# Kernel tuning notes

Hardware: AMD Instinct MI355X
Metric: run time of the kernel (lower is better)

The kernel has to match this reference:

```python
import jax, jax.numpy as jnp
import numpy as np
from jax import lax

NH = 8
DK = 64
DV = 64
IN_C = 64
OUT_C = 128
FH = 32
FW = 32


def conv2d(x, w, b, pad):
    y = lax.conv_general_dilated(x, w, window_strides=(1, 1),
                                 padding=[(pad, pad), (pad, pad)],
                                 dimension_numbers=('NCHW', 'OIHW', 'NCHW'))
    return y + b[None, :, None, None]


def conv1x1(x, w, b):
    # w: [O, C, 1, 1]
    y = jnp.einsum('bchw,oc->bohw', x, w[:, :, 0, 0])
    return y + b[None, :, None, None]


def rel_to_abs(x):
    # x: [B, N, L, 2L-1] -> [B, N, L, L]
    b, n, L, _ = x.shape
    x = jnp.pad(x, ((0, 0), (0, 0), (0, 0), (0, 1)))          # [B,N,L,2L]
    flat = x.reshape(b, n, L * 2 * L)
    flat = jnp.pad(flat, ((0, 0), (0, 0), (0, L - 1)))
    final = flat.reshape(b, n, L + 1, 2 * L - 1)
    return final[:, :, :L, L - 1:]


def relative_logits_1d(q, rel_k, perm):
    # q: [B, Nh, H, W, d]; rel_k: [2W-1, d]
    b, nh, H, W, _ = q.shape
    rel = jnp.einsum('bnxyd,md->bnxym', q, rel_k)              # [B,Nh,H,W,2W-1]
    rel = rel_to_abs(rel.reshape(b, nh * H, W, 2 * W - 1))     # [B,Nh*H,W,W]
    rel = rel.reshape(b, nh, H, 1, W, W)
    rel = jnp.broadcast_to(rel, (b, nh, H, H, W, W))
    rel = jnp.transpose(rel, perm)
    return rel.reshape(b, nh, H * W, H * W)


def augmented_forward(x, conv_w, conv_b, qkv_w, qkv_b, attn_w, attn_b,
                      key_rel_w, key_rel_h):
    b, c, h, w = x.shape
    dkh = DK // NH
    dvh = DV // NH
    hw = h * w

    conv_out = conv2d(x, conv_w, conv_b, pad=1)                # [B, OUT_C-DV, H, W]

    qkv = conv1x1(x, qkv_w, qkv_b)                             # [B, 2DK+DV, H, W]
    q, k, v = jnp.split(qkv, [DK, 2 * DK], axis=1)
    q = q.reshape(b, NH, dkh, h, w) * (dkh ** -0.5)
    k = k.reshape(b, NH, dkh, h, w)
    v = v.reshape(b, NH, dvh, h, w)

    flat_q = q.reshape(b, NH, dkh, hw)
    flat_k = k.reshape(b, NH, dkh, hw)
    flat_v = v.reshape(b, NH, dvh, hw)

    logits = jnp.einsum('bndi,bndj->bnij', flat_q, flat_k)     # [B,Nh,hw,hw]

    q_bnhwd = jnp.transpose(q, (0, 1, 3, 4, 2))                # [B,Nh,H,W,d]
    # width: [B,Nh,H,W,W] broadcast over h2 -> perm to [B,Nh,h,w,h2,w2]
    logits = logits + relative_logits_1d(q_bnhwd, key_rel_w, (0, 1, 2, 4, 3, 5))
    # height: transpose H<->W, perm to [B,Nh,h,w,h2,w2]
    q_t = jnp.transpose(q_bnhwd, (0, 1, 3, 2, 4))
    logits = logits + relative_logits_1d(q_t, key_rel_h, (0, 1, 4, 2, 5, 3))

    weights = jax.nn.softmax(logits, axis=-1)
    attn_out = jnp.einsum('bnij,bndj->bnid', weights, flat_v)  # [B,Nh,hw,dvh]
    attn_out = jnp.transpose(attn_out, (0, 1, 3, 2)).reshape(b, DV, h, w)
    attn_out = conv1x1(attn_out, attn_w, attn_b)
    return jnp.concatenate([conv_out, attn_out], axis=1)


def setup_inputs() -> dict:
    key = jax.random.key(0)
    ks = jax.random.split(key, 10)
    dkh = DK // NH
    return {
        'x': jax.random.normal(ks[0], (8, IN_C, FH, FW), jnp.float32),
        'conv_w': jax.random.normal(ks[1], (OUT_C - DV, IN_C, 3, 3), jnp.float32) * 0.05,
        'conv_b': jnp.zeros((OUT_C - DV,), jnp.float32),
        'qkv_w': jax.random.normal(ks[2], (2 * DK + DV, IN_C, 1, 1), jnp.float32) * 0.05,
        'qkv_b': jnp.zeros((2 * DK + DV,), jnp.float32),
        'attn_w': jax.random.normal(ks[3], (DV, DV, 1, 1), jnp.float32) * 0.05,
        'attn_b': jnp.zeros((DV,), jnp.float32),
        'key_rel_w': jax.random.normal(ks[4], (2 * FW - 1, dkh), jnp.float32) + DK ** -0.5,
        'key_rel_h': jax.random.normal(ks[5], (2 * FH - 1, dkh), jnp.float32) + DK ** -0.5,
    }


def reference(x, conv_w, conv_b, qkv_w, qkv_b, attn_w, attn_b, key_rel_w, key_rel_h):
    return augmented_forward(x, conv_w, conv_b, qkv_w, qkv_b, attn_w, attn_b,
                             key_rel_w, key_rel_h)
```

## Files before the change

kernel.cpp:

```cpp
#include <hip/hip_runtime.h>
#include <hip/hip_bf16.h>
#include <hip/hip_fp16.h>


constexpr int QBUF  = 0;
constexpr int KVBUF = 524288;
constexpr int APRE  = KVBUF + 524288;
constexpr int XT    = APRE + 524288;
constexpr int WT    = XT + 262144;

typedef _Float16 f16x4 __attribute__((ext_vector_type(4)));
typedef _Float16 f16x8 __attribute__((ext_vector_type(8)));
typedef float f32x4 __attribute__((ext_vector_type(4)));

__device__ __forceinline__ float fexp2(float x) {
#if defined(__has_builtin) && __has_builtin(__builtin_amdgcn_exp2f)
    return __builtin_amdgcn_exp2f(x);
#else
    return exp2f(x);
#endif
}

__device__ __forceinline__ float dot8(float4 a, float4 b, const float* r) {
    return a.x*r[0] + a.y*r[1] + a.z*r[2] + a.w*r[3] +
           b.x*r[4] + b.y*r[5] + b.z*r[6] + b.w*r[7];
}

__device__ __forceinline__ f32x4 mfma16x16x32f16(f16x8 a, f16x8 b, f32x4 c) {
    return __builtin_amdgcn_mfma_f32_16x16x32_f16(a, b, c, 0, 0, 0);
}

__device__ __forceinline__ f32x4 mfma16x16x16f16(f16x4 a, f16x4 b, f32x4 c) {
    return __builtin_amdgcn_mfma_f32_16x16x16f16(a, b, c, 0, 0, 0);
}

union PK16 { __half2 hh; unsigned int u; };
union F16V { uint4 u; f16x8 h; };
union F16V4 { uint2 u; f16x4 h; };

constexpr float QSCALE = 0.35355339059327373f * 1.4426950408889634f;

__global__ __launch_bounds__(256) void k_qkv(
    const float* __restrict__ x,
    const float* __restrict__ wq,
    const float* __restrict__ bq,
    const float* __restrict__ wconv,
    float* __restrict__ qbuf,
    unsigned int* __restrict__ kvh,
    unsigned short* __restrict__ xt,
    __half* __restrict__ wt)
{
    int blk = blockIdx.x;
    int tid = threadIdx.x;

    if (blk < 16) {
        int oc0 = blk * 4;
        const float* src = wconv + oc0 * 576;
        #pragma unroll
        for (int j = 0; j < 9; ++j) {
            int local = tid + j * 256;
            float v = src[local];
            int ocr = local / 576, rem = local % 576;
            int ic = rem / 9, tap = rem % 9;
            wt[(oc0 + ocr) * 576 + tap * 64 + ic] = __float2half_rn(v);
        }
        return;
    }

    __shared__ __align__(16) float4 wl4[192];
    __shared__ float bl[12];

    int mblk = blk - 16;
    int b = mblk >> 6, rem = mblk & 63, pc = rem >> 4, og = rem & 15;

    if (tid < 192) wl4[tid] = ((const float4*)(wq + og * 768))[tid];
    if (tid < 12)  bl[tid] = bq[og * 12 + tid];

    int p = pc * 256 + tid;
    const float* xb = x + (b * 64) * 1024 + p;
    float xr[64];
    #pragma unroll
    for (int c = 0; c < 64; ++c) xr[c] = xb[c * 1024];

    __syncthreads();

    for (int pr = 0; pr < 6; ++pr) {
        int oo = pr * 2;
        float accA = bl[oo], accB = bl[oo + 1];
        #pragma unroll
        for (int c4 = 0; c4 < 16; ++c4) {
            float4 wa = wl4[oo * 16 + c4];
            float4 wb = wl4[(oo + 1) * 16 + c4];
            accA = fmaf(wa.x, xr[c4 * 4 + 0], accA);
            accA = fmaf(wa.y, xr[c4 * 4 + 1], accA);
            accA = fmaf(wa.z, xr[c4 * 4 + 2], accA);
            accA = fmaf(wa.w, xr[c4 * 4 + 3], accA);
            accB = fmaf(wb.x, xr[c4 * 4 + 0], accB);
            accB = fmaf(wb.y, xr[c4 * 4 + 1], accB);
            accB = fmaf(wb.z, xr[c4 * 4 + 2], accB);
            accB = fmaf(wb.w, xr[c4 * 4 + 3], accB);
        }
        int o = og * 12 + oo;
        if (o < 64) {
            float2 qv = make_float2(accA * QSCALE, accB * QSCALE);
            *(float2*)(qbuf + ((b * 8 + (o >> 3)) * 1024 + p) * 8 + (o & 7)) = qv;
        } else {
            PK16 pk;
            pk.hh = __floats2half2_rn(accA, accB);
            int idx;
            if (o < 128) {
                int kk = o - 64;
                idx = ((b * 8 + (kk >> 3)) * 1024 + p) * 8 + ((kk & 7) >> 1);
            } else {
                int vv = o - 128;
                idx = ((b * 8 + (vv >> 3)) * 1024 + p) * 8 + 4 + ((vv & 7) >> 1);
            }
            kvh[idx] = pk.u;
        }
    }

    if (og == 0) {
        unsigned int px[32];
        #pragma unroll
        for (int i = 0; i < 32; ++i) {
            PK16 pk;
            pk.hh = __floats2half2_rn(xr[2 * i], xr[2 * i + 1]);
            px[i] = pk.u;
        }
        uint4* dst = (uint4*)(xt + ((size_t)b * 1024 + p) * 64);
        #pragma unroll
        for (int j = 0; j < 8; ++j)
            dst[j] = make_uint4(px[4 * j], px[4 * j + 1], px[4 * j + 2], px[4 * j + 3]);
    }
}

__global__ __launch_bounds__(256) void k_attn(
    const float* __restrict__ qbuf,
    const unsigned int* __restrict__ kvh,
    const float* __restrict__ relw,
    const float* __restrict__ relh,
    float* __restrict__ apre)
{
    __shared__ __align__(16) unsigned char smem[45280];
    unsigned short* Vt  = (unsigned short*)smem;
    unsigned short* Kl  = (unsigned short*)(smem + 18656);
    _Float16*       AHS = (_Float16*)(smem + 35040);

    int tid = threadIdx.x;
    int lane = tid & 63, wv = tid >> 6;
    int bn = blockIdx.x >> 3, qc = blockIdx.x & 7;
    int b = bn >> 3, nh = bn & 7;

    {
        const uint4* kvsrc = (const uint4*)kvh + bn * 2048;
        int p0 = tid * 4;
        #pragma unroll
        for (int pp = 0; pp < 2; ++pp) {
            int pa = p0 + pp * 2;
            uint4 ka = kvsrc[pa * 2 + 0], va = kvsrc[pa * 2 + 1];
            uint4 kb = kvsrc[pa * 2 + 2], vb = kvsrc[pa * 2 + 3];
            *(uint4*)(Kl + pa * 8) = ka;
            *(uint4*)(Kl + pa * 8 + 8) = kb;
            const unsigned short* ha = (const unsigned short*)&va;
            const unsigned short* hb = (const unsigned short*)&vb;
            #pragma unroll
            for (int dv = 0; dv < 8; ++dv) {
                unsigned int pk = (unsigned int)ha[dv] | ((unsigned int)hb[dv] << 16);
                *(unsigned int*)(Vt + dv * 1036 + pa) = pk;
            }
        }
        *(unsigned long long*)(Vt + 8 * 1036 + tid * 4) = 0x3C003C003C003C00ull;
    }

    {
        int qloc = tid >> 1, hh = (tid & 1) * 16;
        int q = qc * 128 + qloc;
        const float* qp = qbuf + (bn * 1024 + q) * 8;
        float4 qa = *(const float4*)qp, qb2 = *(const float4*)(qp + 4);
        int hq = q >> 5;
        #pragma unroll
        for (int m = 0; m < 16; ++m)
            AHS[qloc * 40 + hh + m] =
                (_Float16)dot8(qa, qb2, relh + (hh + m + 31 - hq) * 8);
    }

    int r = lane & 15, g = lane >> 4;
    int qrow0 = wv * 32;
    f16x8 qf[2];
    float awE[2][4], awO[2][4];
    #pragma unroll
    for (int qt = 0; qt < 2; ++qt) {
        int qrow = qrow0 + qt * 16 + r;
        const float* qp = qbuf + (bn * 1024 + qc * 128 + qrow) * 8;
        float4 qa = *(const float4*)qp;
        float4 qb2 = *(const float4*)(qp + 4);
        f16x8 v = {0, 0, 0, 0, 0, 0, 0, 0};
        if (g == 0) {
            v[0] = (_Float16)qa.x; v[1] = (_Float16)qa.y;
            v[2] = (_Float16)qa.z; v[3] = (_Float16)qa.w;
            v[4] = (_Float16)qb2.x; v[5] = (_Float16)qb2.y;
            v[6] = (_Float16)qb2.z; v[7] = (_Float16)qb2.w;
        }
        qf[qt] = v;
        int wq = qrow & 31;
        #pragma unroll
        for (int j = 0; j < 4; ++j) {
            awE[qt][j] = dot8(qa, qb2, relw + (g * 4 + j + 31 - wq) * 8);
            awO[qt][j] = dot8(qa, qb2, relw + (16 + g * 4 + j + 31 - wq) * 8);
        }
    }

    __syncthreads();

    f32x4 acc2[2] = {{0.f, 0.f, 0.f, 0.f}, {0.f, 0.f, 0.f, 0.f}};
    const f32x4 zero = {0.f, 0.f, 0.f, 0.f};

    #pragma unroll 2
    for (int ktp = 0; ktp < 32; ++ktp) {
        int kt0 = ktp * 2;
        F16V kf0, kf1; F16V4 vt0, vt1;
        kf0.u = *(const uint4*)(Kl + (kt0 * 16 + r) * 8);
        kf1.u = *(const uint4*)(Kl + (kt0 * 16 + 16 + r) * 8);
        vt0.u = *(const uint2*)(Vt + r * 1036 + kt0 * 16 + g * 4);
        vt1.u = *(const uint2*)(Vt + r * 1036 + kt0 * 16 + 16 + g * 4);
        #pragma unroll
        for (int qt = 0; qt < 2; ++qt) {
            int qrow = qrow0 + qt * 16 + r;
            float ah = (float)AHS[qrow * 40 + ktp];
            f32x4 a1 = mfma16x16x32f16(kf0.h, qf[qt], zero);
            float e0 = fexp2(a1[0] + awE[qt][0] + ah);
            float e1 = fexp2(a1[1] + awE[qt][1] + ah);
            float e2 = fexp2(a1[2] + awE[qt][2] + ah);
            float e3 = fexp2(a1[3] + awE[qt][3] + ah);
            f16x4 pf;
            pf[0] = (_Float16)e0; pf[1] = (_Float16)e1;
            pf[2] = (_Float16)e2; pf[3] = (_Float16)e3;
            acc2[qt] = mfma16x16x16f16(vt0.h, pf, acc2[qt]);

            f32x4 a2 = mfma16x16x32f16(kf1.h, qf[qt], zero);
            float o0 = fexp2(a2[0] + awO[qt][0] + ah);
            float o1 = fexp2(a2[1] + awO[qt][1] + ah);
            float o2 = fexp2(a2[2] + awO[qt][2] + ah);
            float o3 = fexp2(a2[3] + awO[qt][3] + ah);
            f16x4 pg;
            pg[0] = (_Float16)o0; pg[1] = (_Float16)o1;
            pg[2] = (_Float16)o2; pg[3] = (_Float16)o3;
            acc2[qt] = mfma16x16x16f16(vt1.h, pg, acc2[qt]);
        }
    }

    #pragma unroll
    for (int qt = 0; qt < 2; ++qt) {
        float lsum = __shfl(acc2[qt][0], 32 + r, 64);
        float inv = 1.0f / lsum;
        if (g < 2) {
            int qglob = qc * 128 + qrow0 + qt * 16 + r;
            float* ap = apre + (b * 64 + nh * 8 + g * 4) * 1024 + qglob;
            ap[0]    = acc2[qt][0] * inv;
            ap[1024] = acc2[qt][1] * inv;
            ap[2048] = acc2[qt][2] * inv;
            ap[3072] = acc2[qt][3] * inv;
        }
    }
}

__global__ __launch_bounds__(256) void k_out(
    const unsigned short* __restrict__ xt,
    const unsigned short* __restrict__ wt,
    const float* __restrict__ bconv,
    const float* __restrict__ wattn,
    const float* __restrict__ battn,
    const float* __restrict__ apre,
    float* __restrict__ out)
{
    __shared__ __align__(16) float smem[4352];
    int blk = blockIdx.x;
    int tid = threadIdx.x;

    if (blk < 128) {
        int b = blk >> 4;
        int r0 = (blk & 15) * 2;
        int p0 = r0 * 32;
        int lane = tid & 63, wv = tid >> 6;
        int lr = lane & 15, lk = lane >> 4;
        int n0 = wv * 16;

        F16V bw[18];
        {
            const uint4* wp = (const uint4*)(wt + (n0 + lr) * 576 + lk * 8);
            #pragma unroll
            for (int kk = 0; kk < 18; ++kk) bw[kk].u = wp[kk * 4];
        }

        unsigned char* ats = (unsigned char*)smem;
        {
            const uint4* xsrc = (const uint4*)xt + b * 8192;
            #pragma unroll
            for (int it = 0; it < 5; ++it) {
                int chunk = tid + it * 256;
                if (chunk < 1088) {
                    int s = chunk & 7, cpos = chunk >> 3;
                    int sr = cpos / 34, sc = cpos - sr * 34;
                    int ir = r0 - 1 + sr, icc = sc - 1;
                    uint4 v = make_uint4(0u, 0u, 0u, 0u);
                    if (((unsigned)ir < 32u) && ((unsigned)icc < 32u))
                        v = xsrc[(ir * 32 + icc) * 8 + s];
                    int db = ((sr * 34 + sc) * 128 + s * 16) ^ ((sc & 7) << 4);
                    *(uint4*)(ats + db) = v;
                }
            }
        }
        __syncthreads();

        f32x4 acc[4];
        #pragma unroll
        for (int mb = 0; mb < 4; ++mb) acc[mb] = f32x4{0.f, 0.f, 0.f, 0.f};

        #pragma unroll
        for (int kk = 0; kk < 18; ++kk) {
            const int tap = kk >> 1, h = kk & 1;
            const int dr = tap / 3, dc = tap - dr * 3;
            #pragma unroll
            for (int mb = 0; mb < 4; ++mb) {
                int m = mb * 16 + lr;
                int sr = (m >> 5) + dr, sc = (m & 31) + dc;
                int db = ((sr * 34 + sc) * 128 + h * 64 + lk * 16) ^ ((sc & 7) << 4);
                F16V av;
                av.u = *(const uint4*)(ats + db);
                acc[mb] = __builtin_amdgcn_mfma_f32_16x16x32_f16(av.h, bw[kk].h, acc[mb], 0, 0, 0);
            }
        }

        __syncthreads();
        #pragma unroll
        for (int mb = 0; mb < 4; ++mb) {
            #pragma unroll
            for (int rr = 0; rr < 4; ++rr)
                smem[(mb * 16 + lk * 4 + rr) * 65 + n0 + lr] = acc[mb][rr];
        }
        __syncthreads();

        int oc = tid >> 2, pq = tid & 3;
        float bia = bconv[oc];
        float* op = out + ((b * 128 + oc) * 1024) + p0 + pq * 16;
        #pragma unroll
        for (int j4 = 0; j4 < 4; ++j4) {
            int mloc = pq * 16 + j4 * 4;
            float4 o4;
            o4.x = smem[(mloc + 0) * 65 + oc] + bia;
            o4.y = smem[(mloc + 1) * 65 + oc] + bia;
            o4.z = smem[(mloc + 2) * 65 + oc] + bia;
            o4.w = smem[(mloc + 3) * 65 + oc] + bia;
            *(float4*)(op + j4 * 4) = o4;
        }
    } else {
        int pb = blk - 128;
        int b = pb >> 5, rem = pb & 31, rg = rem >> 3, og = rem & 7;
        int o0 = og * 8;
        float* wl = smem;
        for (int i = tid; i < 512; i += 256) {
            int g = i & 7, c = i >> 3;
            wl[c * 8 + g] = wattn[(o0 + g) * 64 + c];
        }
        if (tid < 8) smem[512 + tid] = battn[o0 + tid];
        __syncthreads();

        int p = rg * 256 + tid;
        float acc[8] = {0, 0, 0, 0, 0, 0, 0, 0};
        const float* ap = apre + b * 65536 + p;
        #pragma unroll 16
        for (int c = 0; c < 64; ++c) {
            float xv = ap[c * 1024];
            const float4* wv4 = (const float4*)(wl + c * 8);
            float4 wa = wv4[0], wb = wv4[1];
            acc[0] = fmaf(wa.x, xv, acc[0]); acc[1] = fmaf(wa.y, xv, acc[1]);
            acc[2] = fmaf(wa.z, xv, acc[2]); acc[3] = fmaf(wa.w, xv, acc[3]);
            acc[4] = fmaf(wb.x, xv, acc[4]); acc[5] = fmaf(wb.y, xv, acc[5]);
            acc[6] = fmaf(wb.z, xv, acc[6]); acc[7] = fmaf(wb.w, xv, acc[7]);
        }
        #pragma unroll
        for (int g = 0; g < 8; ++g)
            out[(b * 128 + 64 + o0 + g) * 1024 + p] = acc[g] + smem[512 + g];
    }
}

extern "C" void kernel_launch(void* const* d_in, const int* in_sizes, int n_in,
                              void* d_out, int out_size, void* d_ws, size_t ws_size,
                              hipStream_t stream)
{
    float* ws = (float*)d_ws;
    float* out = (float*)d_out;
    const float* x      = (const float*)d_in[0];
    const float* conv_w = (const float*)d_in[1];
    const float* conv_b = (const float*)d_in[2];
    const float* qkv_w  = (const float*)d_in[3];
    const float* qkv_b  = (const float*)d_in[4];
    const float* attn_w = (const float*)d_in[5];
    const float* attn_b = (const float*)d_in[6];
    const float* rel_w  = (const float*)d_in[7];
    const float* rel_h  = (const float*)d_in[8];

    k_qkv<<<528, 256, 0, stream>>>(
        x, qkv_w, qkv_b, conv_w,
        ws + QBUF, (unsigned int*)(ws + KVBUF),
        (unsigned short*)(ws + XT), (__half*)(ws + WT));
    k_attn<<<512, 256, 0, stream>>>(
        ws + QBUF, (const unsigned int*)(ws + KVBUF), rel_w, rel_h, ws + APRE);
    k_out<<<384, 256, 0, stream>>>(
        (const unsigned short*)(ws + XT), (const unsigned short*)(ws + WT),
        conv_b, attn_w, attn_b, ws + APRE, out);
}
```

Before: 116.1 us.

## Split attention keys across two blocks and combine partial sums in output kernel

After: 115.9 us. Within noise of the previous version (-0.1%).

```diff
diff --git a/kernel.cpp b/kernel.cpp
--- a/kernel.cpp
+++ b/kernel.cpp
@@ -5,9 +5,11 @@
 
 constexpr int QBUF  = 0;
 constexpr int KVBUF = 524288;
-constexpr int APRE  = KVBUF + 524288;
-constexpr int XT    = APRE + 524288;
-constexpr int WT    = XT + 262144;
+constexpr int APRE0 = 1048576;
+constexpr int APRE1 = 1572864;
+constexpr int LBUF  = 2097152;
+constexpr int XT    = 2228224;
+constexpr int WT    = 2490368;
 
 typedef _Float16 f16x4 __attribute__((ext_vector_type(4)));
 typedef _Float16 f16x8 __attribute__((ext_vector_type(8)));
@@ -139,49 +141,48 @@
     const unsigned int* __restrict__ kvh,
     const float* __restrict__ relw,
     const float* __restrict__ relh,
-    float* __restrict__ apre)
+    float* __restrict__ apre0,
+    float* __restrict__ apre1,
+    float* __restrict__ lbuf)
 {
-    __shared__ __align__(16) unsigned char smem[45280];
+    __shared__ __align__(16) unsigned char smem[22752];
     unsigned short* Vt  = (unsigned short*)smem;
-    unsigned short* Kl  = (unsigned short*)(smem + 18656);
-    _Float16*       AHS = (_Float16*)(smem + 35040);
+    unsigned short* Kl  = (unsigned short*)(smem + 9440);
+    _Float16*       AHS = (_Float16*)(smem + 17632);
 
     int tid = threadIdx.x;
     int lane = tid & 63, wv = tid >> 6;
-    int bn = blockIdx.x >> 3, qc = blockIdx.x & 7;
+    int blk = blockIdx.x;
+    int kh = blk & 1, qc = (blk >> 1) & 7, bn = blk >> 4;
     int b = bn >> 3, nh = bn & 7;
 
     {
-        const uint4* kvsrc = (const uint4*)kvh + bn * 2048;
-        int p0 = tid * 4;
-        #pragma unroll
-        for (int pp = 0; pp < 2; ++pp) {
-            int pa = p0 + pp * 2;
-            uint4 ka = kvsrc[pa * 2 + 0], va = kvsrc[pa * 2 + 1];
-            uint4 kb = kvsrc[pa * 2 + 2], vb = kvsrc[pa * 2 + 3];
-            *(uint4*)(Kl + pa * 8) = ka;
-            *(uint4*)(Kl + pa * 8 + 8) = kb;
-            const unsigned short* ha = (const unsigned short*)&va;
-            const unsigned short* hb = (const unsigned short*)&vb;
-            #pragma unroll
-            for (int dv = 0; dv < 8; ++dv) {
-                unsigned int pk = (unsigned int)ha[dv] | ((unsigned int)hb[dv] << 16);
-                *(unsigned int*)(Vt + dv * 1036 + pa) = pk;
-            }
-        }
-        *(unsigned long long*)(Vt + 8 * 1036 + tid * 4) = 0x3C003C003C003C00ull;
+        const uint4* kvsrc = (const uint4*)kvh + (bn * 1024 + kh * 512) * 2;
+        int pa = tid * 2;
+        uint4 ka = kvsrc[pa * 2 + 0], va = kvsrc[pa * 2 + 1];
+        uint4 kb = kvsrc[pa * 2 + 2], vb = kvsrc[pa * 2 + 3];
+        *(uint4*)(Kl + pa * 8) = ka;
+        *(uint4*)(Kl + pa * 8 + 8) = kb;
+        const unsigned short* ha = (const unsigned short*)&va;
+        const unsigned short* hb = (const unsigned short*)&vb;
+        #pragma unroll
+        for (int dv = 0; dv < 8; ++dv) {
+            unsigned int pk = (unsigned int)ha[dv] | ((unsigned int)hb[dv] << 16);
+            *(unsigned int*)(Vt + dv * 524 + pa) = pk;
+        }
+        *(unsigned int*)(Vt + 8 * 524 + pa) = 0x3C003C00u;
     }
 
     {
-        int qloc = tid >> 1, hh = (tid & 1) * 16;
+        int qloc = tid >> 1, m0 = (tid & 1) * 8;
         int q = qc * 128 + qloc;
         const float* qp = qbuf + (bn * 1024 + q) * 8;
         float4 qa = *(const float4*)qp, qb2 = *(const float4*)(qp + 4);
         int hq = q >> 5;
         #pragma unroll
-        for (int m = 0; m < 16; ++m)
-            AHS[qloc * 40 + hh + m] =
-                (_Float16)dot8(qa, qb2, relh + (hh + m + 31 - hq) * 8);
+        for (int j = 0; j < 8; ++j)
+            AHS[qloc * 20 + m0 + j] =
+                (_Float16)dot8(qa, qb2, relh + (kh * 16 + m0 + j + 31 - hq) * 8);
     }
 
     int r = lane & 15, g = lane >> 4;
@@ -216,17 +217,17 @@
     const f32x4 zero = {0.f, 0.f, 0.f, 0.f};
 
     #pragma unroll 2
-    for (int ktp = 0; ktp < 32; ++ktp) {
+    for (int ktp = 0; ktp < 16; ++ktp) {
         int kt0 = ktp * 2;
         F16V kf0, kf1; F16V4 vt0, vt1;
         kf0.u = *(const uint4*)(Kl + (kt0 * 16 + r) * 8);
         kf1.u = *(const uint4*)(Kl + (kt0 * 16 + 16 + r) * 8);
-        vt0.u = *(const uint2*)(Vt + r * 1036 + kt0 * 16 + g * 4);
-        vt1.u = *(const uint2*)(Vt + r * 1036 + kt0 * 16 + 16 + g * 4);
+        vt0.u = *(const uint2*)(Vt + r * 524 + kt0 * 16 + g * 4);
+        vt1.u = *(const uint2*)(Vt + r * 524 + kt0 * 16 + 16 + g * 4);
         #pragma unroll
         for (int qt = 0; qt < 2; ++qt) {
             int qrow = qrow0 + qt * 16 + r;
-            float ah = (float)AHS[qrow * 40 + ktp];
+            float ah = (float)AHS[qrow * 20 + ktp];
             f32x4 a1 = mfma16x16x32f16(kf0.h, qf[qt], zero);
             float e0 = fexp2(a1[0] + awE[qt][0] + ah);
             float e1 = fexp2(a1[1] + awE[qt][1] + ah);
@@ -249,17 +250,19 @@
         }
     }
 
+    float* aprek = kh ? apre1 : apre0;
     #pragma unroll
     for (int qt = 0; qt < 2; ++qt) {
         float lsum = __shfl(acc2[qt][0], 32 + r, 64);
-        float inv = 1.0f / lsum;
+        int qglob = qc * 128 + qrow0 + qt * 16 + r;
+        if (g == 0)
+            lbuf[(kh * 64 + bn) * 1024 + qglob] = lsum;
         if (g < 2) {
-            int qglob = qc * 128 + qrow0 + qt * 16 + r;
-            float* ap = apre + (b * 64 + nh * 8 + g * 4) * 1024 + qglob;
-            ap[0]    = acc2[qt][0] * inv;
-            ap[1024] = acc2[qt][1] * inv;
-            ap[2048] = acc2[qt][2] * inv;
-            ap[3072] = acc2[qt][3] * inv;
+            float* ap = aprek + (b * 64 + nh * 8 + g * 4) * 1024 + qglob;
+            ap[0]    = acc2[qt][0];
+            ap[1024] = acc2[qt][1];
+            ap[2048] = acc2[qt][2];
+            ap[3072] = acc2[qt][3];
         }
     }
 }
@@ -270,7 +273,9 @@
     const float* __restrict__ bconv,
     const float* __restrict__ wattn,
     const float* __restrict__ battn,
-    const float* __restrict__ apre,
+    const float* __restrict__ apre0,
+    const float* __restrict__ apre1,
+    const float* __restrict__ lbuf,
     float* __restrict__ out)
 {
     __shared__ __align__(16) float smem[4352];
@@ -366,11 +371,21 @@
         __syncthreads();
 
         int p = rg * 256 + tid;
+
+        float inv[8];
+        #pragma unroll
+        for (int nh = 0; nh < 8; ++nh) {
+            float l0 = lbuf[(b * 8 + nh) * 1024 + p];
+            float l1 = lbuf[(64 + b * 8 + nh) * 1024 + p];
+            inv[nh] = 1.0f / (l0 + l1);
+        }
+
         float acc[8] = {0, 0, 0, 0, 0, 0, 0, 0};
-        const float* ap = apre + b * 65536 + p;
-        #pragma unroll 16
+        const float* ap0 = apre0 + b * 65536 + p;
+        const float* ap1 = apre1 + b * 65536 + p;
+        #pragma unroll
         for (int c = 0; c < 64; ++c) {
-            float xv = ap[c * 1024];
+            float xv = (ap0[c * 1024] + ap1[c * 1024]) * inv[c >> 3];
             const float4* wv4 = (const float4*)(wl + c * 8);
             float4 wa = wv4[0], wb = wv4[1];
             acc[0] = fmaf(wa.x, xv, acc[0]); acc[1] = fmaf(wa.y, xv, acc[1]);
@@ -404,9 +419,10 @@
         x, qkv_w, qkv_b, conv_w,
         ws + QBUF, (unsigned int*)(ws + KVBUF),
         (unsigned short*)(ws + XT), (__half*)(ws + WT));
-    k_attn<<<512, 256, 0, stream>>>(
-        ws + QBUF, (const unsigned int*)(ws + KVBUF), rel_w, rel_h, ws + APRE);
+    k_attn<<<1024, 256, 0, stream>>>(
+        ws + QBUF, (const unsigned int*)(ws + KVBUF), rel_w, rel_h,
+        ws + APRE0, ws + APRE1, ws + LBUF);
     k_out<<<384, 256, 0, stream>>>(
         (const unsigned short*)(ws + XT), (const unsigned short*)(ws + WT),
-        conv_b, attn_w, attn_b, ws + APRE, out);
-}
+        conv_b, attn_w, attn_b, ws + APRE0, ws + APRE1, ws + LBUF, out);
+}
```
